# Performance work log

Measured on AMD Instinct MI355X. Metric: run time of the kernel, lower is better.

## Reference

```python
import jax, jax.numpy as jnp
import numpy as np

STATE_DIM = 512
PROJ_DIM = 300


def setup_inputs() -> dict:
    key = jax.random.key(0)
    ks = jax.random.split(key, 10)
    batseq, node_num, edge_num = 320, 32, 1024  # edge_num = node_num**2
    inp = {
        "nodes_feats": jax.random.normal(ks[0], (batseq, node_num, STATE_DIM), jnp.float32),
        "edges_feats": jax.random.normal(ks[1], (batseq, edge_num, STATE_DIM), jnp.float32),
        "adj_mat": jax.random.uniform(ks[2], (batseq, node_num, edge_num), jnp.float32),
        "true_lengths": jax.random.randint(ks[3], (32,), 0, 10),
        "seq_size": 10,
        # Linear layer params (out_features=300, in_features=512), torch layout W: [out, in]
        "W1": jax.random.normal(ks[4], (PROJ_DIM, STATE_DIM), jnp.float32) * 0.02,
        "b1": jnp.zeros((PROJ_DIM,), jnp.float32),
        "W2": jax.random.normal(ks[5], (PROJ_DIM, STATE_DIM), jnp.float32) * 0.02,
        "b2": jnp.zeros((PROJ_DIM,), jnp.float32),
        "W3": jax.random.normal(ks[6], (PROJ_DIM, STATE_DIM), jnp.float32) * 0.02,
        "b3": jnp.zeros((PROJ_DIM,), jnp.float32),
    }
    return inp


def reference(nodes_feats, edges_feats, adj_mat, true_lengths, seq_size,
              W1, b1, W2, b2, W3, b3):
    batseq, node_num, _ = nodes_feats.shape
    batch = batseq // seq_size  # from adj_mat.view(-1, seq_size, node_num, edge_num)
    # Batched replacements for the per-pair tiny Linears
    f1 = jnp.einsum("bnd,pd->bnp", nodes_feats, W1) + b1   # [B, N, 300]
    f3 = jnp.einsum("bnd,pd->bnp", nodes_feats, W3) + b3   # [B, N, 300]
    f2 = jnp.einsum("bed,pd->bep", edges_feats, W2) + b2   # [B, N*N, 300]
    f2 = f2.reshape(batseq, node_num, node_num, PROJ_DIM)  # [B, i, j, 300]
    # per-pair MSE(f_j, f_ij + f_i), mean over (batseq, 300), summed over (i, j)
    diff = f3[:, None, :, :] - f2 - f1[:, :, None, :]
    losses = jnp.sum(diff * diff) / (batseq * PROJ_DIM)
    return losses / batch
```

## Files before the change

### kernel.cpp

```cpp
#include <hip/hip_runtime.h>
#include <hip/hip_bf16.h>
#include <stdint.h>

#define STATE 512
#define PROJ 300
#define PPAD 320
#define BATSEQ 320
#define TE 327680
#define PSTR 328

typedef __bf16 bf16x8 __attribute__((ext_vector_type(8)));
typedef float f32x4 __attribute__((ext_vector_type(4)));

__device__ inline unsigned short f2bf(float x) {
  unsigned u = __builtin_bit_cast(unsigned, x);
  unsigned r = u + 0x7fffu + ((u >> 16) & 1u);
  return (unsigned short)(r >> 16);
}

__global__ __launch_bounds__(256) void prep_kernel(
    const float* __restrict__ W1, const float* __restrict__ b1,
    const float* __restrict__ W2, const float* __restrict__ b2,
    const float* __restrict__ W3, const float* __restrict__ b3,
    unsigned short* __restrict__ w1p, unsigned short* __restrict__ w2p,
    unsigned short* __restrict__ w3p, unsigned short* __restrict__ w2tp,
    float* __restrict__ b1p, float* __restrict__ b2p, float* __restrict__ b3p)
{
  int idx = blockIdx.x * 256 + threadIdx.x;
  const int WN = PPAD * STATE;
  if (idx < 3 * WN) {
    int which = idx / WN, r = idx % WN;
    int cs = r / 512, q = r % 512;
    int lane = q / 8, i = q % 8;
    int c = cs / 16, s = cs % 16;
    int p = c * 16 + (lane & 15);
    int k = s * 32 + (lane >> 4) * 8 + i;
    const float* W = (which == 0) ? W1 : ((which == 1) ? W2 : W3);
    unsigned short* dst = (which == 0) ? w1p : ((which == 1) ? w2p : w3p);
    float v = (p < PROJ) ? W[(size_t)p * STATE + k] : 0.0f;
    dst[r] = f2bf(v);
  } else if (idx < 4 * WN) {
    int r = idx - 3 * WN;
    int cs = r / 512, q = r % 512;
    int lane = q / 8, ii = q % 8;
    int ct = cs / 10, s2 = cs % 10;
    int p = s2 * 32 + (lane >> 4) * 8 + ii;
    int n = ct * 16 + (lane & 15);
    float v = (p < PROJ) ? W2[(size_t)p * STATE + n] : 0.0f;
    w2tp[r] = f2bf(v);
  } else if (idx < 4 * WN + 3 * PPAD) {
    int r = idx - 4 * WN;
    int which = r / PPAD, p = r % PPAD;
    const float* B = (which == 0) ? b1 : ((which == 1) ? b2 : b3);
    float* dst = (which == 0) ? b1p : ((which == 1) ? b2p : b3p);
    dst[p] = (p < PROJ) ? B[p] : 0.0f;
  }
}

__global__ __launch_bounds__(256, 2) void node_kernel(
    const float* __restrict__ nodes,
    const unsigned short* __restrict__ w1p, const unsigned short* __restrict__ w3p,
    const unsigned short* __restrict__ w2tp,
    const float* __restrict__ b1p, const float* __restrict__ b2p,
    const float* __restrict__ b3p,
    float* __restrict__ g1t, float* __restrict__ g3t,
    double* __restrict__ pnode)
{
  __shared__ __align__(16) unsigned short tile[32 * 512];
  __shared__ __align__(16) unsigned short t2a[32 * PSTR];
  __shared__ __align__(16) unsigned short t2b[32 * PSTR];
  __shared__ float G1[PPAD], G3[PPAD];
  __shared__ double red[4];
  const int tid = threadIdx.x;
  const int wave = tid >> 6, lane = tid & 63;
  const int b = blockIdx.x;
  const float* src = nodes + (size_t)b * 32 * STATE;

  for (int t = tid; t < PPAD; t += 256) { G1[t] = 0.f; G3[t] = 0.f; }

  #pragma unroll
  for (int m = 0; m < 16; ++m) {
    int k = wave + 4 * m;
    int row = k >> 1;
    int fc = (k & 1) * 64 + lane;
    f32x4 v = *(const f32x4*)(src + row * STATE + fc * 4);
    unsigned lo = f2bf(v.x) | ((unsigned)f2bf(v.y) << 16);
    unsigned hi = f2bf(v.z) | ((unsigned)f2bf(v.w) << 16);
    unsigned long long pk = (unsigned long long)lo | ((unsigned long long)hi << 32);
    unsigned off = (unsigned)(row * 1024 + fc * 8) ^ (unsigned)((row & 7) << 4);
    *(unsigned long long*)((char*)tile + off) = pk;
  }
  __syncthreads();

  const int lrow = lane & 15, lk = lane >> 4;
  const int cbase = wave * 5;

  f32x4 af1[2][5], af3[2][5];
  #pragma unroll
  for (int rg = 0; rg < 2; ++rg)
    #pragma unroll
    for (int c = 0; c < 5; ++c) {
      af1[rg][c][0]=0.f; af1[rg][c][1]=0.f; af1[rg][c][2]=0.f; af1[rg][c][3]=0.f;
      af3[rg][c][0]=0.f; af3[rg][c][1]=0.f; af3[rg][c][2]=0.f; af3[rg][c][3]=0.f;
    }
  for (int s = 0; s < 16; ++s) {
    bf16x8 a[2];
    #pragma unroll
    for (int rg = 0; rg < 2; ++rg) {
      int row = rg * 16 + lrow;
      unsigned off = (unsigned)(row * 1024 + s * 64 + lk * 16) ^ (unsigned)((row & 7) << 4);
      a[rg] = *(const bf16x8*)((const char*)tile + off);
    }
    #pragma unroll
    for (int c = 0; c < 5; ++c) {
      size_t fo = ((size_t)(((cbase + c) * 16 + s) * 64 + lane)) * 8;
      bf16x8 bf1 = *(const bf16x8*)(w1p + fo);
      bf16x8 bf3 = *(const bf16x8*)(w3p + fo);
      #pragma unroll
      for (int rg = 0; rg < 2; ++rg) {
        af1[rg][c] = __builtin_amdgcn_mfma_f32_16x16x32_bf16(a[rg], bf1, af1[rg][c], 0, 0, 0);
        af3[rg][c] = __builtin_amdgcn_mfma_f32_16x16x32_bf16(a[rg], bf3, af3[rg][c], 0, 0, 0);
      }
    }
  }

  float sq = 0.f;
  #pragma unroll
  for (int rg = 0; rg < 2; ++rg)
    #pragma unroll
    for (int c = 0; c < 5; ++c) {
      int p = (cbase + c) * 16 + lrow;
      float bb1 = b1p[p], bb2 = b2p[p], bb3 = b3p[p];
      #pragma unroll
      for (int r = 0; r < 4; ++r) {
        int m = rg * 16 + lk * 4 + r;
        float v1 = af1[rg][c][r] + bb1;
        float v3 = af3[rg][c][r] + bb3 - bb2;
        t2a[m * PSTR + p] = f2bf(v1);
        t2b[m * PSTR + p] = f2bf(v3);
        sq += v1 * v1 + v3 * v3;
        atomicAdd(&G1[p], v1);
        atomicAdd(&G3[p], v3);
      }
    }
  __syncthreads();

  float s7 = 0.f;
  for (int t = tid; t < PPAD; t += 256) s7 += G3[t] * G1[t];
  float val = 32.f * sq - 2.f * s7;
  #pragma unroll
  for (int m = 32; m >= 1; m >>= 1) val += __shfl_xor(val, m, 64);
  if (lane == 0) red[wave] = (double)val;

  for (int pass = 0; pass < 2; ++pass) {
    const unsigned short* t2 = pass ? t2b : t2a;
    float* gt = pass ? g3t : g1t;
    f32x4 acc2[2][8];
    #pragma unroll
    for (int rg = 0; rg < 2; ++rg)
      #pragma unroll
      for (int cc = 0; cc < 8; ++cc) { acc2[rg][cc][0]=0.f; acc2[rg][cc][1]=0.f; acc2[rg][cc][2]=0.f; acc2[rg][cc][3]=0.f; }
    for (int s2 = 0; s2 < 10; ++s2) {
      bf16x8 a[2];
      #pragma unroll
      for (int rg = 0; rg < 2; ++rg) {
        int mrow = rg * 16 + lrow;
        a[rg] = *(const bf16x8*)(t2 + mrow * PSTR + s2 * 32 + lk * 8);
      }
      #pragma unroll
      for (int cc = 0; cc < 8; ++cc) {
        int ct = wave * 8 + cc;
        bf16x8 bfr = *(const bf16x8*)(w2tp + ((size_t)((ct * 10 + s2) * 64 + lane)) * 8);
        #pragma unroll
        for (int rg = 0; rg < 2; ++rg)
          acc2[rg][cc] = __builtin_amdgcn_mfma_f32_16x16x32_bf16(a[rg], bfr, acc2[rg][cc], 0, 0, 0);
      }
    }
    #pragma unroll
    for (int rg = 0; rg < 2; ++rg)
      #pragma unroll
      for (int cc = 0; cc < 8; ++cc) {
        int n = (wave * 8 + cc) * 16 + lrow;
        #pragma unroll
        for (int r = 0; r < 4; ++r) {
          int mm = rg * 16 + lk * 4 + r;
          gt[((size_t)b * 32 + mm) * STATE + n] = acc2[rg][cc][r];
        }
      }
  }

  __syncthreads();
  if (tid == 0) pnode[b] = red[0] + red[1] + red[2] + red[3];
}

__global__ __launch_bounds__(256, 2) void edge_kernel(
    const float* __restrict__ edges, const unsigned short* __restrict__ w2p,
    const float* __restrict__ g1t, const float* __restrict__ g3t,
    double* __restrict__ pedge)
{
  __shared__ __align__(16) unsigned short tile[64 * 512];
  __shared__ double redd[4][2];
  const int tid = threadIdx.x;
  const int wave = tid >> 6, lane = tid & 63;

  const int orig = blockIdx.x;
  const int wg = (orig & 7) * 640 + (orig >> 3);
  const int b = wg >> 4, q = wg & 15;
  const float* src = edges + ((size_t)b * 1024 + (size_t)q * 64) * STATE;
  const float* g3b = g3t + (size_t)b * 32 * STATE;
  const float* g1b = g1t + ((size_t)b * 32 + (size_t)q * 2) * STATE;

  float cr = 0.f;
  f32x4 sE0 = {0.f, 0.f, 0.f, 0.f}, sE1 = {0.f, 0.f, 0.f, 0.f};
  const int fc = tid & 127;
  const int rhi = tid >> 7;
  #pragma unroll 16
  for (int m = 0; m < 32; ++m) {
    int row = 2 * m + rhi;
    f32x4 e  = *(const f32x4*)(src + row * STATE + fc * 4);
    f32x4 g3 = *(const f32x4*)(g3b + (row & 31) * STATE + fc * 4);
    cr += e.x * g3.x + e.y * g3.y + e.z * g3.z + e.w * g3.w;
    if (m < 16) sE0 += e; else sE1 += e;
    unsigned lo = f2bf(e.x) | ((unsigned)f2bf(e.y) << 16);
    unsigned hi = f2bf(e.z) | ((unsigned)f2bf(e.w) << 16);
    unsigned long long pk = (unsigned long long)lo | ((unsigned long long)hi << 32);
    unsigned off = (unsigned)(row * 1024 + fc * 8) ^ (unsigned)((row & 7) << 4);
    *(unsigned long long*)((char*)tile + off) = pk;
  }
  {
    f32x4 g1a = *(const f32x4*)(g1b + fc * 4);
    f32x4 g1c = *(const f32x4*)(g1b + STATE + fc * 4);
    cr -= sE0.x * g1a.x + sE0.y * g1a.y + sE0.z * g1a.z + sE0.w * g1a.w;
    cr -= sE1.x * g1c.x + sE1.y * g1c.y + sE1.z * g1c.z + sE1.w * g1c.w;
  }
  __syncthreads();

  const int lrow = lane & 15, lk = lane >> 4;
  const int cb = wave * 5;
  f32x4 acc[4][5];
  #pragma unroll
  for (int rg = 0; rg < 4; ++rg)
    #pragma unroll
    for (int c = 0; c < 5; ++c) { acc[rg][c][0]=0.f; acc[rg][c][1]=0.f; acc[rg][c][2]=0.f; acc[rg][c][3]=0.f; }
  for (int s = 0; s < 16; ++s) {
    bf16x8 a[4];
    #pragma unroll
    for (int rg = 0; rg < 4; ++rg) {
      int row = rg * 16 + lrow;
      unsigned off = (unsigned)(row * 1024 + s * 64 + lk * 16) ^ (unsigned)((row & 7) << 4);
      a[rg] = *(const bf16x8*)((const char*)tile + off);
    }
    #pragma unroll
    for (int c = 0; c < 5; ++c) {
      bf16x8 bfr = *(const bf16x8*)(w2p + ((size_t)(((cb + c) * 16 + s) * 64 + lane)) * 8);
      #pragma unroll
      for (int rg = 0; rg < 4; ++rg)
        acc[rg][c] = __builtin_amdgcn_mfma_f32_16x16x32_bf16(a[rg], bfr, acc[rg][c], 0, 0, 0);
    }
  }

  float ss = 0.f;
  #pragma unroll
  for (int rg = 0; rg < 4; ++rg)
    #pragma unroll
    for (int c = 0; c < 5; ++c)
      #pragma unroll
      for (int r = 0; r < 4; ++r) ss += acc[rg][c][r] * acc[rg][c][r];

  #pragma unroll
  for (int m = 32; m >= 1; m >>= 1) {
    ss += __shfl_xor(ss, m, 64);
    cr += __shfl_xor(cr, m, 64);
  }
  if (lane == 0) { redd[wave][0] = (double)ss; redd[wave][1] = (double)cr; }
  __syncthreads();
  if (tid == 0) {
    double sT = 0.0, cT = 0.0;
    #pragma unroll
    for (int w = 0; w < 4; ++w) { sT += redd[w][0]; cT += redd[w][1]; }
    pedge[wg] = sT - 2.0 * cT;
  }
}

__global__ __launch_bounds__(256) void final_kernel(
    const double* __restrict__ pedge, const double* __restrict__ pnode,
    const int* __restrict__ seqp, float* __restrict__ out)
{
  __shared__ double red[4];
  const int tid = threadIdx.x, wave = tid >> 6, lane = tid & 63;
  double v = 0.0;
  for (int t = tid; t < 5120; t += 256) v += pedge[t];
  for (int t = tid; t < 320; t += 256) v += pnode[t];
  #pragma unroll
  for (int m = 32; m >= 1; m >>= 1) v += __shfl_xor(v, m, 64);
  if (lane == 0) red[wave] = v;
  __syncthreads();
  if (tid == 0) {
    double Total = red[0] + red[1] + red[2] + red[3];
    int seq = seqp[0];
    int batch = (seq > 0) ? (BATSEQ / seq) : 1;
    out[0] = (float)(Total / ((double)BATSEQ * (double)PROJ) / (double)batch);
  }
}

extern "C" void kernel_launch(void* const* d_in, const int* in_sizes, int n_in,
                              void* d_out, int out_size, void* d_ws, size_t ws_size,
                              hipStream_t stream)
{
  const float* nodes = (const float*)d_in[0];
  const float* edges = (const float*)d_in[1];
  const int*   seqp  = (const int*)d_in[4];
  const float* W1 = (const float*)d_in[5];
  const float* b1 = (const float*)d_in[6];
  const float* W2 = (const float*)d_in[7];
  const float* b2 = (const float*)d_in[8];
  const float* W3 = (const float*)d_in[9];
  const float* b3 = (const float*)d_in[10];

  char* ws = (char*)d_ws;
  unsigned short* w1p  = (unsigned short*)(ws + 0);
  unsigned short* w3p  = (unsigned short*)(ws + 327680);
  unsigned short* w2p  = (unsigned short*)(ws + 655360);
  unsigned short* w2tp = (unsigned short*)(ws + 983040);
  float* b1p = (float*)(ws + 1310720);
  float* b2p = (float*)(ws + 1312000);
  float* b3p = (float*)(ws + 1313280);
  float* g1t = (float*)(ws + 2097152);
  float* g3t = (float*)(ws + 23068672);
  double* pedge = (double*)(ws + 44040192);
  double* pnode = (double*)(ws + 44081152);

  prep_kernel<<<2564, 256, 0, stream>>>(W1, b1, W2, b2, W3, b3,
                                        w1p, w2p, w3p, w2tp, b1p, b2p, b3p);
  node_kernel<<<320, 256, 0, stream>>>(nodes, w1p, w3p, w2tp, b1p, b2p, b3p,
                                       g1t, g3t, pnode);
  edge_kernel<<<5120, 256, 0, stream>>>(edges, w2p, g1t, g3t, pedge);
  final_kernel<<<1, 256, 0, stream>>>(pedge, pnode, seqp, (float*)d_out);
}
```

Before: 353.3 us.

## Switch edge GEMM to FP8 MFMA and move g3 dot product after GEMM

Edge features and W2 are quantized to FP8 instead of bf16, and the edge GEMM uses the 16x16x32 fp8 MFMA, which halves the LDS tile and the weight fragment bytes. The cross-term with g3 is no longer computed while streaming edges from global memory. It is recomputed afterwards from the FP8 tile in LDS, which removes the g3 global loads from the load loop. The smaller LDS footprint allows 3 blocks per CU. The risk is lower accuracy from FP8 quantization of both the squared-norm and cross terms.

Result: faster. 309.4 us (median of 2 runs) (-12.4%).

```diff
diff --git a/kernel.cpp b/kernel.cpp
--- a/kernel.cpp
+++ b/kernel.cpp
@@ -11,6 +11,8 @@
 
 typedef __bf16 bf16x8 __attribute__((ext_vector_type(8)));
 typedef float f32x4 __attribute__((ext_vector_type(4)));
+typedef float f32x2 __attribute__((ext_vector_type(2)));
+typedef long long i64;
 
 __device__ inline unsigned short f2bf(float x) {
   unsigned u = __builtin_bit_cast(unsigned, x);
@@ -22,25 +24,25 @@
     const float* __restrict__ W1, const float* __restrict__ b1,
     const float* __restrict__ W2, const float* __restrict__ b2,
     const float* __restrict__ W3, const float* __restrict__ b3,
-    unsigned short* __restrict__ w1p, unsigned short* __restrict__ w2p,
-    unsigned short* __restrict__ w3p, unsigned short* __restrict__ w2tp,
+    unsigned short* __restrict__ w1p, unsigned short* __restrict__ w3p,
+    unsigned short* __restrict__ w2tp, unsigned char* __restrict__ w2p8,
     float* __restrict__ b1p, float* __restrict__ b2p, float* __restrict__ b3p)
 {
   int idx = blockIdx.x * 256 + threadIdx.x;
   const int WN = PPAD * STATE;
-  if (idx < 3 * WN) {
+  if (idx < 2 * WN) {
     int which = idx / WN, r = idx % WN;
     int cs = r / 512, q = r % 512;
     int lane = q / 8, i = q % 8;
     int c = cs / 16, s = cs % 16;
     int p = c * 16 + (lane & 15);
     int k = s * 32 + (lane >> 4) * 8 + i;
-    const float* W = (which == 0) ? W1 : ((which == 1) ? W2 : W3);
-    unsigned short* dst = (which == 0) ? w1p : ((which == 1) ? w2p : w3p);
+    const float* W = (which == 0) ? W1 : W3;
+    unsigned short* dst = (which == 0) ? w1p : w3p;
     float v = (p < PROJ) ? W[(size_t)p * STATE + k] : 0.0f;
     dst[r] = f2bf(v);
-  } else if (idx < 4 * WN) {
-    int r = idx - 3 * WN;
+  } else if (idx < 3 * WN) {
+    int r = idx - 2 * WN;
     int cs = r / 512, q = r % 512;
     int lane = q / 8, ii = q % 8;
     int ct = cs / 10, s2 = cs % 10;
@@ -48,6 +50,16 @@
     int n = ct * 16 + (lane & 15);
     float v = (p < PROJ) ? W2[(size_t)p * STATE + n] : 0.0f;
     w2tp[r] = f2bf(v);
+  } else if (idx < 4 * WN) {
+    int r = idx - 3 * WN;
+    int cs = r / 512, q = r % 512;
+    int lane = q / 8, i = q % 8;
+    int c = cs / 16, s = cs % 16;
+    int p = c * 16 + (lane & 15);
+    int k = s * 32 + (lane >> 4) * 8 + i;
+    float v = (p < PROJ) ? W2[(size_t)p * STATE + k] : 0.0f;
+    int pk = __builtin_amdgcn_cvt_pk_fp8_f32(v, 0.f, 0, 0);
+    w2p8[r] = (unsigned char)(pk & 0xff);
   } else if (idx < 4 * WN + 3 * PPAD) {
     int r = idx - 4 * WN;
     int which = r / PPAD, p = r % PPAD;
@@ -193,12 +205,12 @@
   if (tid == 0) pnode[b] = red[0] + red[1] + red[2] + red[3];
 }
 
-__global__ __launch_bounds__(256, 2) void edge_kernel(
-    const float* __restrict__ edges, const unsigned short* __restrict__ w2p,
+__global__ __launch_bounds__(256, 3) void edge_kernel(
+    const float* __restrict__ edges, const unsigned char* __restrict__ w2p8,
     const float* __restrict__ g1t, const float* __restrict__ g3t,
     double* __restrict__ pedge)
 {
-  __shared__ __align__(16) unsigned short tile[64 * 512];
+  __shared__ __align__(16) unsigned char tile[64 * 512];
   __shared__ double redd[4][2];
   const int tid = threadIdx.x;
   const int wave = tid >> 6, lane = tid & 63;
@@ -217,15 +229,12 @@
   #pragma unroll 16
   for (int m = 0; m < 32; ++m) {
     int row = 2 * m + rhi;
-    f32x4 e  = *(const f32x4*)(src + row * STATE + fc * 4);
-    f32x4 g3 = *(const f32x4*)(g3b + (row & 31) * STATE + fc * 4);
-    cr += e.x * g3.x + e.y * g3.y + e.z * g3.z + e.w * g3.w;
+    f32x4 e = *(const f32x4*)(src + row * STATE + fc * 4);
     if (m < 16) sE0 += e; else sE1 += e;
-    unsigned lo = f2bf(e.x) | ((unsigned)f2bf(e.y) << 16);
-    unsigned hi = f2bf(e.z) | ((unsigned)f2bf(e.w) << 16);
-    unsigned long long pk = (unsigned long long)lo | ((unsigned long long)hi << 32);
-    unsigned off = (unsigned)(row * 1024 + fc * 8) ^ (unsigned)((row & 7) << 4);
-    *(unsigned long long*)((char*)tile + off) = pk;
+    int pk = __builtin_amdgcn_cvt_pk_fp8_f32(e.x, e.y, 0, 0);
+    pk = __builtin_amdgcn_cvt_pk_fp8_f32(e.z, e.w, pk, 1);
+    unsigned off = (unsigned)(row * 512 + fc * 4) ^ (unsigned)((row & 7) << 3);
+    *(int*)(tile + off) = pk;
   }
   {
     f32x4 g1a = *(const f32x4*)(g1b + fc * 4);
@@ -243,19 +252,19 @@
     #pragma unroll
     for (int c = 0; c < 5; ++c) { acc[rg][c][0]=0.f; acc[rg][c][1]=0.f; acc[rg][c][2]=0.f; acc[rg][c][3]=0.f; }
   for (int s = 0; s < 16; ++s) {
-    bf16x8 a[4];
+    i64 a[4];
     #pragma unroll
     for (int rg = 0; rg < 4; ++rg) {
       int row = rg * 16 + lrow;
-      unsigned off = (unsigned)(row * 1024 + s * 64 + lk * 16) ^ (unsigned)((row & 7) << 4);
-      a[rg] = *(const bf16x8*)((const char*)tile + off);
+      unsigned off = (unsigned)(row * 512 + s * 32 + lk * 8) ^ (unsigned)((row & 7) << 3);
+      a[rg] = *(const i64*)(tile + off);
     }
     #pragma unroll
     for (int c = 0; c < 5; ++c) {
-      bf16x8 bfr = *(const bf16x8*)(w2p + ((size_t)(((cb + c) * 16 + s) * 64 + lane)) * 8);
+      i64 bfr = *(const i64*)(w2p8 + ((size_t)(((cb + c) * 16 + s) * 64 + lane)) * 8);
       #pragma unroll
       for (int rg = 0; rg < 4; ++rg)
-        acc[rg][c] = __builtin_amdgcn_mfma_f32_16x16x32_bf16(a[rg], bfr, acc[rg][c], 0, 0, 0);
+        acc[rg][c] = __builtin_amdgcn_mfma_f32_16x16x32_fp8_fp8(a[rg], bfr, acc[rg][c], 0, 0, 0);
     }
   }
 
@@ -266,6 +275,37 @@
     for (int c = 0; c < 5; ++c)
       #pragma unroll
       for (int r = 0; r < 4; ++r) ss += acc[rg][c][r] * acc[rg][c][r];
+
+  {
+    const int j = tid >> 3, s8 = tid & 7;
+    const float* g3r = g3b + (size_t)j * STATE + s8 * 64;
+    const unsigned sw = (unsigned)((j & 7) << 3);
+    float part = 0.f;
+    #pragma unroll
+    for (int c = 0; c < 8; ++c) {
+      unsigned o0 = (unsigned)(j * 512 + s8 * 64 + c * 8) ^ sw;
+      unsigned o1 = (unsigned)((j + 32) * 512 + s8 * 64 + c * 8) ^ sw;
+      i64 p0 = *(const i64*)(tile + o0);
+      i64 p1 = *(const i64*)(tile + o1);
+      int l0 = (int)(p0 & 0xffffffffll), h0 = (int)(((unsigned long long)p0) >> 32);
+      int l1 = (int)(p1 & 0xffffffffll), h1 = (int)(((unsigned long long)p1) >> 32);
+      f32x2 a0 = __builtin_amdgcn_cvt_pk_f32_fp8(l0, 0);
+      f32x2 a1 = __builtin_amdgcn_cvt_pk_f32_fp8(l0, 1);
+      f32x2 a2 = __builtin_amdgcn_cvt_pk_f32_fp8(h0, 0);
+      f32x2 a3 = __builtin_amdgcn_cvt_pk_f32_fp8(h0, 1);
+      f32x2 c0 = __builtin_amdgcn_cvt_pk_f32_fp8(l1, 0);
+      f32x2 c1 = __builtin_amdgcn_cvt_pk_f32_fp8(l1, 1);
+      f32x2 c2 = __builtin_amdgcn_cvt_pk_f32_fp8(h1, 0);
+      f32x2 c3 = __builtin_amdgcn_cvt_pk_f32_fp8(h1, 1);
+      f32x4 g0 = *(const f32x4*)(g3r + c * 8);
+      f32x4 g1v = *(const f32x4*)(g3r + c * 8 + 4);
+      part += (a0.x + c0.x) * g0.x + (a0.y + c0.y) * g0.y
+            + (a1.x + c1.x) * g0.z + (a1.y + c1.y) * g0.w
+            + (a2.x + c2.x) * g1v.x + (a2.y + c2.y) * g1v.y
+            + (a3.x + c3.x) * g1v.z + (a3.y + c3.y) * g1v.w;
+    }
+    cr += part;
+  }
 
   #pragma unroll
   for (int m = 32; m >= 1; m >>= 1) {
@@ -320,20 +360,20 @@
   char* ws = (char*)d_ws;
   unsigned short* w1p  = (unsigned short*)(ws + 0);
   unsigned short* w3p  = (unsigned short*)(ws + 327680);
-  unsigned short* w2p  = (unsigned short*)(ws + 655360);
-  unsigned short* w2tp = (unsigned short*)(ws + 983040);
-  float* b1p = (float*)(ws + 1310720);
-  float* b2p = (float*)(ws + 1312000);
-  float* b3p = (float*)(ws + 1313280);
+  unsigned short* w2tp = (unsigned short*)(ws + 655360);
+  unsigned char*  w2p8 = (unsigned char*)(ws + 983040);
+  float* b1p = (float*)(ws + 1146880);
+  float* b2p = (float*)(ws + 1148160);
+  float* b3p = (float*)(ws + 1149440);
   float* g1t = (float*)(ws + 2097152);
   float* g3t = (float*)(ws + 23068672);
   double* pedge = (double*)(ws + 44040192);
   double* pnode = (double*)(ws + 44081152);
 
   prep_kernel<<<2564, 256, 0, stream>>>(W1, b1, W2, b2, W3, b3,
-                                        w1p, w2p, w3p, w2tp, b1p, b2p, b3p);
+                                        w1p, w3p, w2tp, w2p8, b1p, b2p, b3p);
   node_kernel<<<320, 256, 0, stream>>>(nodes, w1p, w3p, w2tp, b1p, b2p, b3p,
                                        g1t, g3t, pnode);
-  edge_kernel<<<5120, 256, 0, stream>>>(edges, w2p, g1t, g3t, pedge);
+  edge_kernel<<<5120, 256, 0, stream>>>(edges, w2p8, g1t, g3t, pedge);
   final_kernel<<<1, 256, 0, stream>>>(pedge, pnode, seqp, (float*)d_out);
 }
```
